# Kernel optimization log

Measured on AMD Instinct MI355X. Metric: run time of the kernel, lower is better.

Reference implementation:

```python
import jax, jax.numpy as jnp
import numpy as np

V, D, L, S = 32000, 512, 4096, 256
LOG2 = float(np.log(2.0))


def _self_conflict(a, span):
    # a: [S, l] bool. Sequential: a[i] = a[i] & ~a[i-1] (using updated values).
    def step1(prev, cur):
        out = cur & ~prev
        return out, out
    first = a[:, 0]
    _, rest = jax.lax.scan(step1, first, a[:, 1:].T)  # scan over token axis
    a = jnp.concatenate([first[:, None], rest.T], axis=1)
    if span == 3:
        # second pass: a[i] = a[i] & ~a[i-2] on the updated array
        def step2(carry, cur):
            pm2, pm1 = carry
            out = cur & ~pm2
            return (pm1, out), out
        _, rest2 = jax.lax.scan(step2, (a[:, 0], a[:, 1]), a[:, 2:].T)
        a = jnp.concatenate([a[:, :2], rest2.T], axis=1)
    return a


def _shift_into(a1, off, L2):
    # hit[j] |= a1[j - off], zeros elsewhere
    B, l1 = a1.shape
    out = jnp.zeros((B, L2), dtype=bool)
    if off >= 0:
        end = min(L2, off + l1)
        return out.at[:, off:end].set(a1[:, :end - off])
    return out.at[:, :l1 + off].set(a1[:, -off:])


def _intersec_conflict(a1, a2, flag=False):
    # a2[j] cleared if any overlapping a1 span is active (set of shifts)
    l1, l2 = a1.shape[1], a2.shape[1]
    hit = jnp.zeros_like(a2)
    for i in range(l2 - l1 + 1):
        hit = hit | _shift_into(a1, i, l2)
    if flag:
        hit = hit | _shift_into(a1, -1, l2) | _shift_into(a1, 2, l2)
    return a2 & ~hit


def _forward(x, embd, w1, b1, w2, b2, w3, b3, g1, g2, g3, align1, align2, align3):
    emb = embd[x]                                   # [1, L, D]
    s2 = (emb[:, 1:] + emb[:, :-1]) / 2             # [1, L-1, D]
    s3 = (emb[:, 2:] + emb[:, 1:-1] + emb[:, :-2]) / 3
    heads = ((emb, w1, b1, g1, align1), (s2, w2, b2, g2, align2), (s3, w3, b3, g3, align3))
    stats, bools = [], []
    for spans, w, b, g, amask in heads:
        logits = spans @ w + b                      # [1, l, 2]
        logp = jax.nn.log_softmax(logits, axis=-1)
        p = jnp.exp(logp)
        nent = -(p * logp).sum(-1) / LOG2           # normalized entropy (2 classes)
        idx = jnp.argmax(logp + g, axis=-1)         # [S, l] Gumbel-max categorical sample
        act = jax.nn.one_hot(idx, 2, dtype=logp.dtype)
        bools.append((idx == 0) & amask[None, :])   # reduce chosen AND aligned
        stats.append((logp, nent, act))

    b1_, b2_, b3_ = bools
    b3_ = _self_conflict(b3_, 3)
    b2_ = _intersec_conflict(b3_, b2_, flag=True)
    b1_ = _intersec_conflict(b3_, b1_)
    b2_ = _self_conflict(b2_, 2)
    b1_ = _intersec_conflict(b2_, b1_)

    logp1, ne1, act1 = stats[0]
    logp2, ne2, _ = stats[1]
    logp3, ne3, _ = stats[2]
    # actions 2/3 are rewritten from the conflict-reduced booleans; action 1 keeps its sample
    act2 = jnp.stack([b2_, ~b2_], axis=-1).astype(logp2.dtype)
    act3 = jnp.stack([b3_, ~b3_], axis=-1).astype(logp3.dtype)

    nll1 = -(act1 * logp1).sum(-1).sum(1)           # [S]
    nll2 = -(act2 * logp2).sum(-1).sum(1)
    nll3 = -(act3 * logp3).sum(-1).sum(1)
    nsamp = act1.shape[0]
    nent = jnp.broadcast_to((ne1.mean(1) + ne2.mean(1) + ne3.mean(1)) / 3.0, (nsamp,))
    return nent, nll1 + nll2 + nll3, b1_, b2_, b3_


def setup_inputs():
    key = jax.random.key(0)
    k = jax.random.split(key, 11)
    x = jax.random.randint(k[0], (1, L), 0, V)
    embd = jax.random.normal(k[1], (V, D), jnp.float32) * 0.02
    w1 = jax.random.normal(k[2], (D, 2), jnp.float32) * 0.05
    w2 = jax.random.normal(k[3], (D, 2), jnp.float32) * 0.05
    w3 = jax.random.normal(k[4], (D, 2), jnp.float32) * 0.05
    b1 = jnp.zeros((2,), jnp.float32)
    b2 = jnp.zeros((2,), jnp.float32)
    b3 = jnp.zeros((2,), jnp.float32)
    g1 = jax.random.gumbel(k[5], (S, L, 2), jnp.float32)
    g2 = jax.random.gumbel(k[6], (S, L - 1, 2), jnp.float32)
    g3 = jax.random.gumbel(k[7], (S, L - 2, 2), jnp.float32)
    align1 = jax.random.randint(k[8], (L,), 0, 2).astype(bool)
    align2 = jax.random.randint(k[9], (L - 1,), 0, 2).astype(bool)
    align3 = jax.random.randint(k[10], (L - 2,), 0, 2).astype(bool)
    return {"x": x, "sample_num": S, "align1": align1, "align2": align2, "align3": align3,
            "embd": embd, "w1": w1, "b1": b1, "w2": w2, "b2": b2, "w3": w3, "b3": b3,
            "g1": g1, "g2": g2, "g3": g3}


def reference(x, sample_num, align1, align2, align3, embd, w1, b1, w2, b2, w3, b3, g1, g2, g3):
    return _forward(x, embd, w1, b1, w2, b2, w3, b3, g1, g2, g3, align1, align2, align3)
```

## Files before the change

### kernel.cpp

```cpp
#include <hip/hip_runtime.h>
#include <stdint.h>

#define L_ 4096
#define S_ 256
#define D_ 512
#define NW 64

static __device__ const float LN2F = 0.69314718055994530942f;

__global__ __launch_bounds__(256)
void k_rows(const int* __restrict__ x, const float* __restrict__ embd,
            const float* __restrict__ w1, const float* __restrict__ b1,
            const float* __restrict__ w2, const float* __restrict__ b2,
            const float* __restrict__ w3, const float* __restrict__ b3,
            float2* __restrict__ lph, float* __restrict__ entbuf) {
    const int wid  = threadIdx.x >> 6;
    const int lane = threadIdx.x & 63;
    const int t = blockIdx.x * 4 + wid;
    const int t1 = (t + 1 < L_) ? t + 1 : t;
    const int t2 = (t + 2 < L_) ? t + 2 : t;
    const int d0 = lane * 8;

    const float4* e0p = (const float4*)(embd + (size_t)x[t]  * D_ + d0);
    const float4* e1p = (const float4*)(embd + (size_t)x[t1] * D_ + d0);
    const float4* e2p = (const float4*)(embd + (size_t)x[t2] * D_ + d0);
    float4 e0a = e0p[0], e0b = e0p[1];
    float4 e1a = e1p[0], e1b = e1p[1];
    float4 e2a = e2p[0], e2b = e2p[1];
    const float4* w1p = (const float4*)(w1 + 2 * d0);
    const float4* w2p = (const float4*)(w2 + 2 * d0);
    const float4* w3p = (const float4*)(w3 + 2 * d0);

    float v0[8] = {e0a.x,e0a.y,e0a.z,e0a.w,e0b.x,e0b.y,e0b.z,e0b.w};
    float v1[8] = {e1a.x,e1a.y,e1a.z,e1a.w,e1b.x,e1b.y,e1b.z,e1b.w};
    float v2[8] = {e2a.x,e2a.y,e2a.z,e2a.w,e2b.x,e2b.y,e2b.z,e2b.w};
    float wv1[16], wv2[16], wv3[16];
    for (int q = 0; q < 4; q++) {
        float4 a = w1p[q]; wv1[4*q]=a.x; wv1[4*q+1]=a.y; wv1[4*q+2]=a.z; wv1[4*q+3]=a.w;
        float4 b = w2p[q]; wv2[4*q]=b.x; wv2[4*q+1]=b.y; wv2[4*q+2]=b.z; wv2[4*q+3]=b.w;
        float4 c = w3p[q]; wv3[4*q]=c.x; wv3[4*q+1]=c.y; wv3[4*q+2]=c.z; wv3[4*q+3]=c.w;
    }
    double a0=0,a1=0,a2=0,a3=0,a4=0,a5=0;
    #pragma unroll
    for (int j = 0; j < 8; j++) {
        float s2 = (v1[j] + v0[j]) * 0.5f;
        float s3 = ((v2[j] + v1[j]) + v0[j]) / 3.0f;
        a0 += (double)v0[j] * (double)wv1[2*j];
        a1 += (double)v0[j] * (double)wv1[2*j+1];
        a2 += (double)s2    * (double)wv2[2*j];
        a3 += (double)s2    * (double)wv2[2*j+1];
        a4 += (double)s3    * (double)wv3[2*j];
        a5 += (double)s3    * (double)wv3[2*j+1];
    }
    #pragma unroll
    for (int o = 32; o > 0; o >>= 1) {
        a0 += __shfl_xor(a0, o, 64);
        a1 += __shfl_xor(a1, o, 64);
        a2 += __shfl_xor(a2, o, 64);
        a3 += __shfl_xor(a3, o, 64);
        a4 += __shfl_xor(a4, o, 64);
        a5 += __shfl_xor(a5, o, 64);
    }
    if (lane < 3) {
        double l0, l1; const float* bb;
        if (lane == 0)      { l0 = a0; l1 = a1; bb = b1; }
        else if (lane == 1) { l0 = a2; l1 = a3; bb = b2; }
        else                { l0 = a4; l1 = a5; bb = b3; }
        bool valid = (lane == 0) || (lane == 1 && t < L_-1) || (lane == 2 && t < L_-2);
        float ev = 0.0f;
        if (valid) {
            l0 += (double)bb[0]; l1 += (double)bb[1];
            double m = fmax(l0, l1);
            double sa = l0 - m, sb = l1 - m;
            double lse = log(exp(sa) + exp(sb));
            float p0l = (float)(sa - lse), p1l = (float)(sb - lse);
            lph[lane*L_ + t] = make_float2(p0l, p1l);
            float p0 = expf(p0l), p1 = expf(p1l);
            ev = -(p0*p0l + p1*p1l) / LN2F;
        }
        entbuf[lane*L_ + t] = ev;
    }
}

__device__ __forceinline__ uint64_t pass1_noc(uint64_t wp) {
    uint64_t o = wp & ~(wp << 1);
    uint64_t h = wp & (wp << 1);
    o |= (o << 2)  & h; h &= (h << 2);
    o |= (o << 4)  & h; h &= (h << 4);
    o |= (o << 8)  & h; h &= (h << 8);
    o |= (o << 16) & h; h &= (h << 16);
    o |= (o << 32) & h;
    return o;
}
__device__ __forceinline__ uint64_t pass2_noc(uint64_t ap) {
    uint64_t o = ap & ~(ap << 2);
    uint64_t h = ap & (ap << 2);
    o |= (o << 4)  & h; h &= (h << 4);
    o |= (o << 8)  & h; h &= (h << 8);
    o |= (o << 16) & h; h &= (h << 16);
    o |= (o << 32) & h;
    return o;
}

__global__ __launch_bounds__(1024)
void k_fused(const float2* __restrict__ lph,
             const int* __restrict__ al1, const int* __restrict__ al2, const int* __restrict__ al3,
             const float2* __restrict__ g1, const float2* __restrict__ g2, const float2* __restrict__ g3,
             const float* __restrict__ entbuf, float* __restrict__ out) {
    const int s = blockIdx.x;
    const int tid = threadIdx.x;
    const int lane = tid & 63;
    const int wv = tid >> 6;

    __shared__ uint64_t w1s[NW], w2s[NW], w3s[NW];
    __shared__ uint64_t o1s[NW], o2s[NW], o3s[NW];

    float2 lph2v[4], lph3v[4];
    float nllacc = 0.0f;
    #pragma unroll
    for (int it = 0; it < 4; it++) {
        const int t = it * 1024 + tid;
        float2 v1 = g1[(size_t)s * L_ + t];
        float2 p1v = lph[t];
        bool raw1 = (p1v.x + v1.x) >= (p1v.y + v1.y);
        bool m1 = raw1 && (al1[t] != 0);
        nllacc += raw1 ? -p1v.x : -p1v.y;
        bool m2 = false, m3 = false;
        lph2v[it] = make_float2(0.f, 0.f);
        lph3v[it] = make_float2(0.f, 0.f);
        if (t < L_-1) {
            float2 v2 = g2[(size_t)s * (L_-1) + t];
            float2 p2v = lph[L_ + t];
            lph2v[it] = p2v;
            m2 = ((p2v.x + v2.x) >= (p2v.y + v2.y)) && (al2[t] != 0);
        }
        if (t < L_-2) {
            float2 v3 = g3[(size_t)s * (L_-2) + t];
            float2 p3v = lph[2*L_ + t];
            lph3v[it] = p3v;
            m3 = ((p3v.x + v3.x) >= (p3v.y + v3.y)) && (al3[t] != 0);
        }
        unsigned long long b1b = __ballot(m1);
        unsigned long long b2b = __ballot(m2);
        unsigned long long b3b = __ballot(m3);
        if (lane == 0) {
            int w = t >> 6;
            w1s[w] = b1b; w2s[w] = b2b; w3s[w] = b3b;
        }
    }
    __syncthreads();

    if (wv == 0) {
        const int j = lane;
        uint64_t w3w = w3s[j];
        uint64_t oA = pass1_noc(w3w);
        uint64_t oB = pass1_noc(w3w & ~1ull);
        unsigned F = (unsigned)(oA >> 63) | (((unsigned)(oB >> 63)) << 1);
        #pragma unroll
        for (int d = 1; d < 64; d <<= 1) {
            unsigned P = __shfl_up(F, d, 64);
            if (lane >= d) {
                unsigned la = P & 1, lb = (P >> 1) & 1;
                unsigned ra = F & 1, rb = (F >> 1) & 1;
                F = (la ? rb : ra) | ((lb ? rb : ra) << 1);
            }
        }
        unsigned Fp = __shfl_up(F, 1, 64);
        unsigned cin = (lane == 0) ? 0u : (Fp & 1);
        uint64_t p1 = cin ? oB : oA;

        uint64_t q0 = pass2_noc(p1);
        uint64_t q1 = pass2_noc(p1 & ~1ull);
        uint64_t q2 = pass2_noc(p1 & ~2ull);
        uint64_t q3 = pass2_noc(p1 & ~3ull);
        #define ST_(o) ((unsigned)(((o >> 62) & 1) | (((o >> 63) & 1) << 1)))
        unsigned G = ST_(q0) | (ST_(q1) << 2) | (ST_(q2) << 4) | (ST_(q3) << 6);
        #undef ST_
        #pragma unroll
        for (int d = 1; d < 64; d <<= 1) {
            unsigned P = __shfl_up(G, d, 64);
            if (lane >= d) {
                unsigned H = 0;
                #pragma unroll
                for (int xx = 0; xx < 4; xx++) {
                    unsigned m = (P >> (2 * xx)) & 3;
                    H |= ((G >> (2 * m)) & 3) << (2 * xx);
                }
                G = H;
            }
        }
        unsigned Gp = __shfl_up(G, 1, 64);
        unsigned s2in = (lane == 0) ? 0u : (Gp & 3);
        uint64_t B3 = (s2in == 0) ? q0 : (s2in == 1) ? q1 : (s2in == 2) ? q2 : q3;

        uint64_t B3m1 = __shfl_up((unsigned long long)B3, 1, 64); if (lane == 0)  B3m1 = 0;
        uint64_t B3nx = __shfl_down((unsigned long long)B3, 1, 64); if (lane == 63) B3nx = 0;
        uint64_t sh1 = (B3 << 1) | (B3m1 >> 63);
        uint64_t sh2 = (B3 << 2) | (B3m1 >> 62);
        uint64_t shm = (B3 >> 1) | (B3nx << 63);
        uint64_t hit2 = B3 | sh1 | sh2 | shm;

        uint64_t in2 = w2s[j] & ~hit2;
        uint64_t oA2 = pass1_noc(in2);
        uint64_t oB2 = pass1_noc(in2 & ~1ull);
        unsigned F2 = (unsigned)(oA2 >> 63) | (((unsigned)(oB2 >> 63)) << 1);
        #pragma unroll
        for (int d = 1; d < 64; d <<= 1) {
            unsigned P = __shfl_up(F2, d, 64);
            if (lane >= d) {
                unsigned la = P & 1, lb = (P >> 1) & 1;
                unsigned ra = F2 & 1, rb = (F2 >> 1) & 1;
                F2 = (la ? rb : ra) | ((lb ? rb : ra) << 1);
            }
        }
        unsigned F2p = __shfl_up(F2, 1, 64);
        unsigned cin2 = (lane == 0) ? 0u : (F2p & 1);
        uint64_t B2 = cin2 ? oB2 : oA2;

        uint64_t B2m1 = __shfl_up((unsigned long long)B2, 1, 64); if (lane == 0) B2m1 = 0;
        uint64_t hit1 = B3 | sh1 | sh2 | B2 | ((B2 << 1) | (B2m1 >> 63));
        uint64_t B1 = w1s[j] & ~hit1;

        o1s[j] = B1; o2s[j] = B2; o3s[j] = B3;
    }
    __syncthreads();

    float* b1o = out + 2*S_;
    float* b2o = b1o + (size_t)S_ * L_;
    float* b3o = b2o + (size_t)S_ * (L_-1);
    #pragma unroll
    for (int it = 0; it < 4; it++) {
        const int t = it * 1024 + tid;
        const int w = t >> 6, b = t & 63;
        b1o[(size_t)s*L_ + t] = (float)((o1s[w] >> b) & 1);
        if (t < L_-1) {
            unsigned bit = (unsigned)((o2s[w] >> b) & 1);
            b2o[(size_t)s*(L_-1) + t] = (float)bit;
            nllacc += bit ? -lph2v[it].x : -lph2v[it].y;
        }
        if (t < L_-2) {
            unsigned bit = (unsigned)((o3s[w] >> b) & 1);
            b3o[(size_t)s*(L_-2) + t] = (float)bit;
            nllacc += bit ? -lph3v[it].x : -lph3v[it].y;
        }
    }
    #pragma unroll
    for (int o = 32; o > 0; o >>= 1) nllacc += __shfl_xor(nllacc, o, 64);
    __shared__ float red[16];
    if (lane == 0) red[wv] = nllacc;
    __syncthreads();
    if (tid == 0) {
        float tot = 0.f;
        #pragma unroll
        for (int i = 0; i < 16; i++) tot += red[i];
        out[S_ + s] = tot;
    }

    if (s == 0 && wv == 0) {
        double s1 = 0, s2d = 0, s3d = 0;
        for (int t = lane; t < L_; t += 64) {
            s1  += (double)entbuf[t];
            s2d += (double)entbuf[L_ + t];
            s3d += (double)entbuf[2*L_ + t];
        }
        #pragma unroll
        for (int o = 32; o > 0; o >>= 1) {
            s1  += __shfl_xor(s1, o, 64);
            s2d += __shfl_xor(s2d, o, 64);
            s3d += __shfl_xor(s3d, o, 64);
        }
        float v = (float)((s1 / (double)L_ + s2d / (double)(L_-1) + s3d / (double)(L_-2)) / 3.0);
        #pragma unroll
        for (int i = 0; i < 4; i++) out[lane + 64*i] = v;
    }
}

extern "C" void kernel_launch(void* const* d_in, const int* in_sizes, int n_in,
                              void* d_out, int out_size, void* d_ws, size_t ws_size,
                              hipStream_t stream) {
    const int*   x    = (const int*)d_in[0];
    const int*   al1  = (const int*)d_in[2];
    const int*   al2  = (const int*)d_in[3];
    const int*   al3  = (const int*)d_in[4];
    const float* embd = (const float*)d_in[5];
    const float* w1   = (const float*)d_in[6];
    const float* b1   = (const float*)d_in[7];
    const float* w2   = (const float*)d_in[8];
    const float* b2   = (const float*)d_in[9];
    const float* w3   = (const float*)d_in[10];
    const float* b3   = (const float*)d_in[11];
    const float2* g1  = (const float2*)d_in[12];
    const float2* g2  = (const float2*)d_in[13];
    const float2* g3  = (const float2*)d_in[14];
    float* out = (float*)d_out;

    float2* lph   = (float2*)d_ws;
    float* entbuf = (float*)(lph + 3 * L_);

    hipLaunchKernelGGL(k_rows, dim3(1024), dim3(256), 0, stream,
                       x, embd, w1, b1, w2, b2, w3, b3, lph, entbuf);
    hipLaunchKernelGGL(k_fused, dim3(S_), dim3(1024), 0, stream,
                       lph, al1, al2, al3, g1, g2, g3, entbuf, out);
}
```

Before: 168.6 us.

## Vectorize fused kernel to two tokens per thread and scan redundantly per wave

Each thread now handles two adjacent tokens, using float4 and int2 loads for the Gumbel noise, log-probs and alignment masks, and float2 stores for the outputs. Even and odd ballots are interleaved into 64-bit words with a bit-spread helper. Every wave now runs the sequential-conflict scan itself instead of only wave 0, which removes the second __syncthreads and the o*s shared arrays. Each wave then reads its output words from the scan result by cross-lane shuffle. The cost is redundant bit-scan work in all 16 waves and scalar, misaligned access for the g2 and b2 rows.

```diff
diff --git a/kernel.cpp b/kernel.cpp
--- a/kernel.cpp
+++ b/kernel.cpp
@@ -101,6 +101,18 @@
     o |= (o << 32) & h;
     return o;
 }
+__device__ __forceinline__ uint64_t p1b1(uint64_t x) {
+    x &= 0xFFFFFFFFull;
+    x = (x | (x << 16)) & 0x0000FFFF0000FFFFull;
+    x = (x | (x << 8))  & 0x00FF00FF00FF00FFull;
+    x = (x | (x << 4))  & 0x0F0F0F0F0F0F0F0Full;
+    x = (x | (x << 2))  & 0x3333333333333333ull;
+    x = (x | (x << 1))  & 0x5555555555555555ull;
+    return x;
+}
+__device__ __forceinline__ uint64_t shfl_u64(uint64_t v, int src) {
+    return (uint64_t)__shfl((unsigned long long)v, src, 64);
+}
 
 __global__ __launch_bounds__(1024)
 void k_fused(const float2* __restrict__ lph,
@@ -113,135 +125,157 @@
     const int wv = tid >> 6;
 
     __shared__ uint64_t w1s[NW], w2s[NW], w3s[NW];
-    __shared__ uint64_t o1s[NW], o2s[NW], o3s[NW];
-
-    float2 lph2v[4], lph3v[4];
+
+    const float2* g1s = g1 + (size_t)s * L_;
+    const float2* g2s = g2 + (size_t)s * (L_-1);
+    const float2* g3s = g3 + (size_t)s * (L_-2);
+
+    float4 lp2v[2], lp3v[2];
     float nllacc = 0.0f;
-    #pragma unroll
-    for (int it = 0; it < 4; it++) {
-        const int t = it * 1024 + tid;
-        float2 v1 = g1[(size_t)s * L_ + t];
-        float2 p1v = lph[t];
-        bool raw1 = (p1v.x + v1.x) >= (p1v.y + v1.y);
-        bool m1 = raw1 && (al1[t] != 0);
-        nllacc += raw1 ? -p1v.x : -p1v.y;
-        bool m2 = false, m3 = false;
-        lph2v[it] = make_float2(0.f, 0.f);
-        lph3v[it] = make_float2(0.f, 0.f);
-        if (t < L_-1) {
-            float2 v2 = g2[(size_t)s * (L_-1) + t];
-            float2 p2v = lph[L_ + t];
-            lph2v[it] = p2v;
-            m2 = ((p2v.x + v2.x) >= (p2v.y + v2.y)) && (al2[t] != 0);
-        }
-        if (t < L_-2) {
-            float2 v3 = g3[(size_t)s * (L_-2) + t];
-            float2 p3v = lph[2*L_ + t];
-            lph3v[it] = p3v;
-            m3 = ((p3v.x + v3.x) >= (p3v.y + v3.y)) && (al3[t] != 0);
-        }
-        unsigned long long b1b = __ballot(m1);
-        unsigned long long b2b = __ballot(m2);
-        unsigned long long b3b = __ballot(m3);
+
+    #pragma unroll
+    for (int it = 0; it < 2; it++) {
+        const int q = it * 1024 + tid;
+        float4 gg1 = ((const float4*)g1s)[q];
+        float4 pp1 = ((const float4*)lph)[q];
+        int2   aa1 = ((const int2*)al1)[q];
+        bool r1e = (pp1.x + gg1.x) >= (pp1.y + gg1.y);
+        bool r1o = (pp1.z + gg1.z) >= (pp1.w + gg1.w);
+        bool m1e = r1e && (aa1.x != 0);
+        bool m1o = r1o && (aa1.y != 0);
+        nllacc += (r1e ? -pp1.x : -pp1.y) + (r1o ? -pp1.z : -pp1.w);
+
+        bool m2e = false, m2o = false, m3e = false, m3o = false;
+        float4 p2 = make_float4(0.f,0.f,0.f,0.f), p3 = make_float4(0.f,0.f,0.f,0.f);
+        if (q < 2047) {
+            float2 ga = g2s[2*q], gb = g2s[2*q+1];
+            p2 = ((const float4*)(lph + L_))[q];
+            int2 aa2 = ((const int2*)al2)[q];
+            m2e = ((p2.x + ga.x) >= (p2.y + ga.y)) && (aa2.x != 0);
+            m2o = ((p2.z + gb.x) >= (p2.w + gb.y)) && (aa2.y != 0);
+            float4 gg3 = ((const float4*)g3s)[q];
+            p3 = ((const float4*)(lph + 2*L_))[q];
+            int2 aa3 = ((const int2*)al3)[q];
+            m3e = ((p3.x + gg3.x) >= (p3.y + gg3.y)) && (aa3.x != 0);
+            m3o = ((p3.z + gg3.z) >= (p3.w + gg3.w)) && (aa3.y != 0);
+        } else {
+            float2 ga = g2s[4094];
+            float2 pa = lph[L_ + 4094];
+            p2 = make_float4(pa.x, pa.y, 0.f, 0.f);
+            m2e = ((pa.x + ga.x) >= (pa.y + ga.y)) && (al2[4094] != 0);
+        }
+        lp2v[it] = p2; lp3v[it] = p3;
+
+        uint64_t be1 = __ballot(m1e), bo1 = __ballot(m1o);
+        uint64_t be2 = __ballot(m2e), bo2 = __ballot(m2o);
+        uint64_t be3 = __ballot(m3e), bo3 = __ballot(m3o);
+        const int w0i = it * 32 + wv * 2;
         if (lane == 0) {
-            int w = t >> 6;
-            w1s[w] = b1b; w2s[w] = b2b; w3s[w] = b3b;
+            w1s[w0i] = p1b1(be1) | (p1b1(bo1) << 1);
+            w2s[w0i] = p1b1(be2) | (p1b1(bo2) << 1);
+            w3s[w0i] = p1b1(be3) | (p1b1(bo3) << 1);
+        } else if (lane == 1) {
+            w1s[w0i+1] = p1b1(be1 >> 32) | (p1b1(bo1 >> 32) << 1);
+            w2s[w0i+1] = p1b1(be2 >> 32) | (p1b1(bo2 >> 32) << 1);
+            w3s[w0i+1] = p1b1(be3 >> 32) | (p1b1(bo3 >> 32) << 1);
         }
     }
     __syncthreads();
 
-    if (wv == 0) {
-        const int j = lane;
-        uint64_t w3w = w3s[j];
-        uint64_t oA = pass1_noc(w3w);
-        uint64_t oB = pass1_noc(w3w & ~1ull);
-        unsigned F = (unsigned)(oA >> 63) | (((unsigned)(oB >> 63)) << 1);
-        #pragma unroll
-        for (int d = 1; d < 64; d <<= 1) {
-            unsigned P = __shfl_up(F, d, 64);
-            if (lane >= d) {
-                unsigned la = P & 1, lb = (P >> 1) & 1;
-                unsigned ra = F & 1, rb = (F >> 1) & 1;
-                F = (la ? rb : ra) | ((lb ? rb : ra) << 1);
+    const int j = lane;
+    uint64_t w3w = w3s[j];
+    uint64_t oA = pass1_noc(w3w);
+    uint64_t oB = pass1_noc(w3w & ~1ull);
+    unsigned F = (unsigned)(oA >> 63) | (((unsigned)(oB >> 63)) << 1);
+    #pragma unroll
+    for (int d = 1; d < 64; d <<= 1) {
+        unsigned P = __shfl_up(F, d, 64);
+        if (lane >= d) {
+            unsigned la = P & 1, lb = (P >> 1) & 1;
+            unsigned ra = F & 1, rb = (F >> 1) & 1;
+            F = (la ? rb : ra) | ((lb ? rb : ra) << 1);
+        }
+    }
+    unsigned Fp = __shfl_up(F, 1, 64);
+    unsigned cin = (lane == 0) ? 0u : (Fp & 1);
+    uint64_t p1w_ = cin ? oB : oA;
+
+    uint64_t q0 = pass2_noc(p1w_);
+    uint64_t q1 = pass2_noc(p1w_ & ~1ull);
+    uint64_t q2 = pass2_noc(p1w_ & ~2ull);
+    uint64_t q3 = pass2_noc(p1w_ & ~3ull);
+    #define ST_(o) ((unsigned)(((o >> 62) & 1) | (((o >> 63) & 1) << 1)))
+    unsigned G = ST_(q0) | (ST_(q1) << 2) | (ST_(q2) << 4) | (ST_(q3) << 6);
+    #undef ST_
+    #pragma unroll
+    for (int d = 1; d < 64; d <<= 1) {
+        unsigned P = __shfl_up(G, d, 64);
+        if (lane >= d) {
+            unsigned H = 0;
+            #pragma unroll
+            for (int xx = 0; xx < 4; xx++) {
+                unsigned m = (P >> (2 * xx)) & 3;
+                H |= ((G >> (2 * m)) & 3) << (2 * xx);
             }
-        }
-        unsigned Fp = __shfl_up(F, 1, 64);
-        unsigned cin = (lane == 0) ? 0u : (Fp & 1);
-        uint64_t p1 = cin ? oB : oA;
-
-        uint64_t q0 = pass2_noc(p1);
-        uint64_t q1 = pass2_noc(p1 & ~1ull);
-        uint64_t q2 = pass2_noc(p1 & ~2ull);
-        uint64_t q3 = pass2_noc(p1 & ~3ull);
-        #define ST_(o) ((unsigned)(((o >> 62) & 1) | (((o >> 63) & 1) << 1)))
-        unsigned G = ST_(q0) | (ST_(q1) << 2) | (ST_(q2) << 4) | (ST_(q3) << 6);
-        #undef ST_
-        #pragma unroll
-        for (int d = 1; d < 64; d <<= 1) {
-            unsigned P = __shfl_up(G, d, 64);
-            if (lane >= d) {
-                unsigned H = 0;
-                #pragma unroll
-                for (int xx = 0; xx < 4; xx++) {
-                    unsigned m = (P >> (2 * xx)) & 3;
-                    H |= ((G >> (2 * m)) & 3) << (2 * xx);
-                }
-                G = H;
-            }
-        }
-        unsigned Gp = __shfl_up(G, 1, 64);
-        unsigned s2in = (lane == 0) ? 0u : (Gp & 3);
-        uint64_t B3 = (s2in == 0) ? q0 : (s2in == 1) ? q1 : (s2in == 2) ? q2 : q3;
-
-        uint64_t B3m1 = __shfl_up((unsigned long long)B3, 1, 64); if (lane == 0)  B3m1 = 0;
-        uint64_t B3nx = __shfl_down((unsigned long long)B3, 1, 64); if (lane == 63) B3nx = 0;
-        uint64_t sh1 = (B3 << 1) | (B3m1 >> 63);
-        uint64_t sh2 = (B3 << 2) | (B3m1 >> 62);
-        uint64_t shm = (B3 >> 1) | (B3nx << 63);
-        uint64_t hit2 = B3 | sh1 | sh2 | shm;
-
-        uint64_t in2 = w2s[j] & ~hit2;
-        uint64_t oA2 = pass1_noc(in2);
-        uint64_t oB2 = pass1_noc(in2 & ~1ull);
-        unsigned F2 = (unsigned)(oA2 >> 63) | (((unsigned)(oB2 >> 63)) << 1);
-        #pragma unroll
-        for (int d = 1; d < 64; d <<= 1) {
-            unsigned P = __shfl_up(F2, d, 64);
-            if (lane >= d) {
-                unsigned la = P & 1, lb = (P >> 1) & 1;
-                unsigned ra = F2 & 1, rb = (F2 >> 1) & 1;
-                F2 = (la ? rb : ra) | ((lb ? rb : ra) << 1);
-            }
-        }
-        unsigned F2p = __shfl_up(F2, 1, 64);
-        unsigned cin2 = (lane == 0) ? 0u : (F2p & 1);
-        uint64_t B2 = cin2 ? oB2 : oA2;
-
-        uint64_t B2m1 = __shfl_up((unsigned long long)B2, 1, 64); if (lane == 0) B2m1 = 0;
-        uint64_t hit1 = B3 | sh1 | sh2 | B2 | ((B2 << 1) | (B2m1 >> 63));
-        uint64_t B1 = w1s[j] & ~hit1;
-
-        o1s[j] = B1; o2s[j] = B2; o3s[j] = B3;
-    }
-    __syncthreads();
-
-    float* b1o = out + 2*S_;
-    float* b2o = b1o + (size_t)S_ * L_;
-    float* b3o = b2o + (size_t)S_ * (L_-1);
-    #pragma unroll
-    for (int it = 0; it < 4; it++) {
-        const int t = it * 1024 + tid;
-        const int w = t >> 6, b = t & 63;
-        b1o[(size_t)s*L_ + t] = (float)((o1s[w] >> b) & 1);
-        if (t < L_-1) {
-            unsigned bit = (unsigned)((o2s[w] >> b) & 1);
-            b2o[(size_t)s*(L_-1) + t] = (float)bit;
-            nllacc += bit ? -lph2v[it].x : -lph2v[it].y;
-        }
-        if (t < L_-2) {
-            unsigned bit = (unsigned)((o3s[w] >> b) & 1);
-            b3o[(size_t)s*(L_-2) + t] = (float)bit;
-            nllacc += bit ? -lph3v[it].x : -lph3v[it].y;
+            G = H;
+        }
+    }
+    unsigned Gp = __shfl_up(G, 1, 64);
+    unsigned s2in = (lane == 0) ? 0u : (Gp & 3);
+    uint64_t B3 = (s2in == 0) ? q0 : (s2in == 1) ? q1 : (s2in == 2) ? q2 : q3;
+
+    uint64_t B3m1 = shfl_u64(B3, lane - 1); if (lane == 0)  B3m1 = 0;
+    uint64_t B3nx = shfl_u64(B3, lane + 1); if (lane == 63) B3nx = 0;
+    uint64_t sh1 = (B3 << 1) | (B3m1 >> 63);
+    uint64_t sh2 = (B3 << 2) | (B3m1 >> 62);
+    uint64_t shm = (B3 >> 1) | (B3nx << 63);
+    uint64_t hit2 = B3 | sh1 | sh2 | shm;
+
+    uint64_t in2 = w2s[j] & ~hit2;
+    uint64_t oA2 = pass1_noc(in2);
+    uint64_t oB2 = pass1_noc(in2 & ~1ull);
+    unsigned F2 = (unsigned)(oA2 >> 63) | (((unsigned)(oB2 >> 63)) << 1);
+    #pragma unroll
+    for (int d = 1; d < 64; d <<= 1) {
+        unsigned P = __shfl_up(F2, d, 64);
+        if (lane >= d) {
+            unsigned la = P & 1, lb = (P >> 1) & 1;
+            unsigned ra = F2 & 1, rb = (F2 >> 1) & 1;
+            F2 = (la ? rb : ra) | ((lb ? rb : ra) << 1);
+        }
+    }
+    unsigned F2p = __shfl_up(F2, 1, 64);
+    unsigned cin2 = (lane == 0) ? 0u : (F2p & 1);
+    uint64_t B2 = cin2 ? oB2 : oA2;
+
+    uint64_t B2m1 = shfl_u64(B2, lane - 1); if (lane == 0) B2m1 = 0;
+    uint64_t hit1 = B3 | sh1 | sh2 | B2 | ((B2 << 1) | (B2m1 >> 63));
+    uint64_t B1 = w1s[j] & ~hit1;
+
+    float2* b1r = (float2*)(out + 2*S_ + (size_t)s*L_);
+    float*  b2r = out + 2*S_ + (size_t)S_*L_ + (size_t)s*(L_-1);
+    float2* b3r = (float2*)(out + 2*S_ + (size_t)S_*L_ + (size_t)S_*(L_-1) + (size_t)s*(L_-2));
+    #pragma unroll
+    for (int it = 0; it < 2; it++) {
+        const int q = it * 1024 + tid;
+        const int widx = it * 32 + wv * 2 + (lane >> 5);
+        const int bp = 2 * (lane & 31);
+        uint64_t W1 = shfl_u64(B1, widx);
+        uint64_t W2 = shfl_u64(B2, widx);
+        uint64_t W3 = shfl_u64(B3, widx);
+        unsigned v1e = (unsigned)(W1 >> bp) & 1, v1o = (unsigned)(W1 >> bp >> 1) & 1;
+        unsigned v2e = (unsigned)(W2 >> bp) & 1, v2o = (unsigned)(W2 >> bp >> 1) & 1;
+        unsigned v3e = (unsigned)(W3 >> bp) & 1, v3o = (unsigned)(W3 >> bp >> 1) & 1;
+        b1r[q] = make_float2((float)v1e, (float)v1o);
+        if (q < 2047) {
+            b2r[2*q]   = (float)v2e;
+            b2r[2*q+1] = (float)v2o;
+            nllacc += (v2e ? -lp2v[it].x : -lp2v[it].y) + (v2o ? -lp2v[it].z : -lp2v[it].w);
+            b3r[q] = make_float2((float)v3e, (float)v3o);
+            nllacc += (v3e ? -lp3v[it].x : -lp3v[it].y) + (v3o ? -lp3v[it].z : -lp3v[it].w);
+        } else {
+            b2r[4094] = (float)v2e;
+            nllacc += (v2e ? -lp2v[it].x : -lp2v[it].y);
         }
     }
     #pragma unroll
```

Result: no change. 166.9 us (-1.0%).
